# Kernel optimization log

Measured on AMD Instinct MI355X. Metric: run time of the kernel, lower is better.

## Reference

```python
import jax, jax.numpy as jnp
import numpy as np

B, S, HID = 2, 2048, 2048
H, HK, D = 32, 8, 64
N_REP = H // HK
SCALE = D ** -0.5


def setup_inputs() -> dict:
    key = jax.random.key(0)
    ks = jax.random.split(key, 9)
    std = HID ** -0.5
    causal = jnp.tril(jnp.ones((S, S), dtype=bool))
    attention_mask = jnp.where(causal, 0.0, -1e9).astype(jnp.float32)[None, None]  # [1,1,S,S]
    return {
        "hidden_states": jax.random.normal(ks[0], (B, S, HID), jnp.float32),
        "attention_mask": attention_mask,
        "q_w": jax.random.normal(ks[1], (HID, H * D), jnp.float32) * std,
        "q_b": jax.random.normal(ks[2], (H * D,), jnp.float32) * 0.01,
        "k_w": jax.random.normal(ks[3], (HID, HK * D), jnp.float32) * std,
        "k_b": jax.random.normal(ks[4], (HK * D,), jnp.float32) * 0.01,
        "v_w": jax.random.normal(ks[5], (HID, HK * D), jnp.float32) * std,
        "v_b": jax.random.normal(ks[6], (HK * D,), jnp.float32) * 0.01,
        "dense_w": jax.random.normal(ks[7], (HID, HID), jnp.float32) * std,
        "dense_b": jax.random.normal(ks[8], (HID,), jnp.float32) * 0.01,
    }


def reference(hidden_states, attention_mask, q_w, q_b, k_w, k_b, v_w, v_b, dense_w, dense_b):
    b, s, _ = hidden_states.shape
    # projections -> [b, h, s, d]
    q = (hidden_states @ q_w + q_b).reshape(b, s, H, D).transpose(0, 2, 1, 3)
    k = (hidden_states @ k_w + k_b).reshape(b, s, HK, D).transpose(0, 2, 1, 3)
    v = (hidden_states @ v_w + v_b).reshape(b, s, HK, D).transpose(0, 2, 1, 3)
    # GQA: repeat_kv (repeat_interleave along head dim)
    k = jnp.repeat(k, N_REP, axis=1)  # [b, H, s, d]
    v = jnp.repeat(v, N_REP, axis=1)
    # eager attention: full score matrix
    scores = jnp.einsum("bhqd,bhkd->bhqk", q, k) * SCALE + attention_mask
    w = jax.nn.softmax(scores.astype(jnp.float32), axis=-1).astype(q.dtype)
    attn = jnp.einsum("bhqk,bhkd->bhqd", w, v)
    attn = attn.transpose(0, 2, 1, 3).reshape(b, s, H * D)
    return attn @ dense_w + dense_b
```

## Files before the change

kernel.cpp:

```cpp
#include <hip/hip_runtime.h>
#include <hip/hip_bf16.h>


typedef short s16x8 __attribute__((ext_vector_type(8)));
typedef float f32x4 __attribute__((ext_vector_type(4)));

static constexpr int BB = 2, SS = 2048, HID = 2048, HH = 32, HKV = 8, DD = 64;
static constexpr int MM = BB * SS;
static constexpr int NQKV = 3072;

#define DEV __device__ __forceinline__

DEV short f2bf(float f) {
    unsigned u = __builtin_bit_cast(unsigned, f);
    return (short)((u + 0x7fffu + ((u >> 16) & 1u)) >> 16);
}

DEV void stage16(const short* gsrc, short* lbase) {
    __builtin_amdgcn_global_load_lds((const __attribute__((address_space(1))) void*)gsrc,
                                     (__attribute__((address_space(3))) void*)lbase, 16, 0, 0);
}

__global__ __launch_bounds__(256) void cvt_f32_bf16(const float* __restrict__ in,
                                                    short* __restrict__ out, int n) {
    int i = (blockIdx.x * 256 + threadIdx.x) * 8;
    if (i >= n) return;
    float4 a = *reinterpret_cast<const float4*>(in + i);
    float4 b = *reinterpret_cast<const float4*>(in + i + 4);
    s16x8 o;
    o[0] = f2bf(a.x); o[1] = f2bf(a.y); o[2] = f2bf(a.z); o[3] = f2bf(a.w);
    o[4] = f2bf(b.x); o[5] = f2bf(b.y); o[6] = f2bf(b.z); o[7] = f2bf(b.w);
    *reinterpret_cast<s16x8*>(out + i) = o;
}

__global__ __launch_bounds__(256) void transpose_cvt(const float* __restrict__ in,
                                                     short* __restrict__ out,
                                                     int K, int N) {
    __shared__ float tile[32][33];
    int k0 = blockIdx.x * 32, n0 = blockIdx.y * 32;
    int tx = threadIdx.x & 31, ty = threadIdx.x >> 5;
#pragma unroll
    for (int r = ty; r < 32; r += 8)
        tile[r][tx] = in[(size_t)(k0 + r) * N + n0 + tx];
    __syncthreads();
#pragma unroll
    for (int r = ty; r < 32; r += 8)
        out[(size_t)(n0 + r) * K + k0 + tx] = f2bf(tile[tx][r]);
}

__global__ __launch_bounds__(256) void transpose_v(const short* __restrict__ QKV,
                                                   short* __restrict__ Vtg) {
    __shared__ int tile[32][33];
    const int s0 = blockIdx.x * 32, c0 = blockIdx.y * 32, b = blockIdx.z;
    const int tx = threadIdx.x & 31, ty = threadIdx.x >> 5;
#pragma unroll
    for (int r = ty; r < 32; r += 8)
        tile[r][tx] = QKV[(size_t)(b * SS + s0 + r) * NQKV + 2560 + c0 + tx];
    __syncthreads();
#pragma unroll
    for (int r = ty; r < 32; r += 8) {
        const int c = c0 + r;
        Vtg[((size_t)(b * HKV + (c >> 6)) * 64 + (c & 63)) * SS + s0 + tx] = (short)tile[tx][r];
    }
}

__global__ __launch_bounds__(256) void concat_bias(const float* __restrict__ qb,
                                                   const float* __restrict__ kb,
                                                   const float* __restrict__ vb,
                                                   float* __restrict__ cb) {
    int i = blockIdx.x * 256 + threadIdx.x;
    if (i < 2048) cb[i] = qb[i];
    else if (i < 2560) cb[i] = kb[i - 2048];
    else if (i < 3072) cb[i] = vb[i - 2560];
}

template <int BM, int BN, typename OutT>
__global__ __launch_bounds__(512) void gemm8p(const short* __restrict__ A,
                                              const short* __restrict__ Bt,
                                              const float* __restrict__ bias,
                                              OutT* __restrict__ C,
                                              int M, int N, int K, int qcols) {
    constexpr int NR = BN / 64;
    constexpr int ACH = BM * 4;
    constexpr int BCH = BN * 4;
    static_assert(ACH % 512 == 0, "A chunks per half must be thread-uniform");
    constexpr int SA = ACH / 512;
    __shared__ __align__(16) short lds[(BM + BN) * 128];
    const int tid = threadIdx.x, lane = tid & 63, wid = tid >> 6;
    const int fr = lane & 15, fk = lane >> 4;
    const int wm = wid >> 2, wn = wid & 3;
    const int nbn = N / BN;
    const int cpx = gridDim.x >> 3;
    const int wg = (blockIdx.x & 7) * cpx + (blockIdx.x >> 3);
    const int bm = wg / nbn, bn = wg % nbn;
    const int NT = K / 64;

    const short* Ablk = A + (size_t)bm * BM * K;
    const short* Bblk = Bt + (size_t)bn * BN * K;

    auto abase = [&](int bf, int kh) { return bf * (BM * 64) + kh * (BM * 32); };
    auto bbase = [&](int bf, int kh) { return 2 * (BM * 64) + bf * (BN * 64) + kh * (BN * 32); };

    auto stA = [&](int bf, int kh, int kt) {
#pragma unroll
        for (int l = 0; l < SA; ++l) {
            const int c = l * 512 + tid;
            const int r = c >> 2, sg = (c & 3) ^ ((r >> 1) & 3);
            stage16(Ablk + (size_t)r * K + kt + kh * 32 + sg * 8,
                    &lds[abase(bf, kh) + (l * 512 + wid * 64) * 8]);
        }
    };
    auto stB = [&](int bf, int kh, int kt) {
        {
            const int c = tid;
            const int r = c >> 2, sg = (c & 3) ^ ((r >> 1) & 3);
            stage16(Bblk + (size_t)r * K + kt + kh * 32 + sg * 8,
                    &lds[bbase(bf, kh) + (wid * 64) * 8]);
        }
        if constexpr (BCH > 512) {
            if (tid < BCH - 512) {
                const int c = 512 + tid;
                const int r = c >> 2, sg = (c & 3) ^ ((r >> 1) & 3);
                stage16(Bblk + (size_t)r * K + kt + kh * 32 + sg * 8,
                        &lds[bbase(bf, kh) + ((512 + wid * 64)) * 8]);
            }
        }
    };

    auto waithalf = [&](bool pf) {
        if (!pf) { asm volatile("s_waitcnt vmcnt(0)" ::: "memory"); return; }
        if constexpr (BCH > 512) {
            if (wid < (BCH - 512) / 64) asm volatile("s_waitcnt vmcnt(4)" ::: "memory");
            else                        asm volatile("s_waitcnt vmcnt(3)" ::: "memory");
        } else {
            asm volatile("s_waitcnt vmcnt(3)" ::: "memory");
        }
    };

    f32x4 acc[8][NR] = {};

    stA(0, 0, 0); stB(0, 0, 0);
    stA(0, 1, 0); stB(0, 1, 0);
    waithalf(true);
    asm volatile("s_barrier" ::: "memory");

    for (int t = 0; t < NT; ++t) {
        const int bf = t & 1, sf = bf ^ 1;
        const int ktn = (t + 1) * 64;
        const bool pf = (t + 1 < NT);
#pragma unroll
        for (int kh = 0; kh < 2; ++kh) {
            s16x8 bfrag[NR], afrag[8];
#pragma unroll
            for (int n = 0; n < NR; ++n) {
                const int row = wn * (BN / 4) + n * 16 + fr;
                bfrag[n] = *reinterpret_cast<const s16x8*>(
                    &lds[bbase(bf, kh) + row * 32 + ((fk ^ ((row >> 1) & 3)) * 8)]);
            }
#pragma unroll
            for (int i = 0; i < 8; ++i) {
                const int row = wm * 128 + i * 16 + fr;
                afrag[i] = *reinterpret_cast<const s16x8*>(
                    &lds[abase(bf, kh) + row * 32 + ((fk ^ ((row >> 1) & 3)) * 8)]);
            }
            if (pf) stA(sf, kh, ktn);
            __builtin_amdgcn_s_setprio(1);
#pragma unroll
            for (int i = 0; i < 4; ++i)
#pragma unroll
                for (int n = 0; n < NR; ++n)
                    acc[i][n] = __builtin_amdgcn_mfma_f32_16x16x32_bf16(
                        afrag[i], bfrag[n], acc[i][n], 0, 0, 0);
            __builtin_amdgcn_s_setprio(0);
            if (pf) stB(sf, kh, ktn);
            __builtin_amdgcn_s_setprio(1);
#pragma unroll
            for (int i = 4; i < 8; ++i)
#pragma unroll
                for (int n = 0; n < NR; ++n)
                    acc[i][n] = __builtin_amdgcn_mfma_f32_16x16x32_bf16(
                        afrag[i], bfrag[n], acc[i][n], 0, 0, 0);
            __builtin_amdgcn_s_setprio(0);
            waithalf(pf);
            asm volatile("s_barrier" ::: "memory");
        }
    }

#pragma unroll
    for (int n = 0; n < NR; ++n) {
        const int col = bn * BN + wn * (BN / 4) + n * 16 + fr;
        const float bv = bias[col];
        const float sc = (col < qcols) ? 0.125f : 1.0f;
#pragma unroll
        for (int mi = 0; mi < 8; ++mi) {
            const int row0 = bm * BM + wm * 128 + mi * 16 + fk * 4;
#pragma unroll
            for (int r = 0; r < 4; ++r) {
                const float v = (acc[mi][n][r] + bv) * sc;
                if constexpr (sizeof(OutT) == 2)
                    reinterpret_cast<short*>(C)[(size_t)(row0 + r) * N + col] = f2bf(v);
                else
                    reinterpret_cast<float*>(C)[(size_t)(row0 + r) * N + col] = v;
            }
        }
    }
}

__global__ __launch_bounds__(256, 2) void attn_fwd(
        const short* __restrict__ QKV,
        const short* __restrict__ Vtg,
        short* __restrict__ Ob) {
    constexpr int KB = 64;
    __shared__ __align__(16) short Qs[128 * 64];
    __shared__ __align__(16) short Ks[2][KB * 64];
    __shared__ __align__(16) short Vt[2][64 * 64];
    __shared__ __align__(16) short Ps[128 * 64];

    const int pair = blockIdx.x;
    const int bh = blockIdx.y;
    const int b = bh >> 5, h = bh & 31;
    const int kvh = h >> 2;
    const int tid = threadIdx.x, lane = tid & 63, wid = tid >> 6;
    const int fr = lane & 15, fk = lane >> 4;
    const int wq0 = wid * 32;

    const short* kbase = QKV + (size_t)b * SS * NQKV + 2048 + kvh * DD;
    const short* vbase = Vtg + (size_t)(b * HKV + kvh) * 64 * SS;

    auto stageKV = [&](int bb, int kv0) {
#pragma unroll
        for (int is = 0; is < 2; ++is) {
            const int c = is * 256 + wid * 64 + lane;
            const int r = c >> 3, sg = (c & 7) ^ (r & 7);
            stage16(kbase + (size_t)(kv0 + r) * NQKV + sg * 8,
                    &Ks[bb][(is * 256 + wid * 64) * 8]);
            stage16(vbase + (size_t)r * SS + kv0 + sg * 8,
                    &Vt[bb][(is * 256 + wid * 64) * 8]);
        }
    };
    auto stageQ = [&](int q0) {
        const short* qbase = QKV + ((size_t)b * SS + q0) * NQKV + h * DD;
#pragma unroll
        for (int is = 0; is < 4; ++is) {
            const int c = is * 256 + wid * 64 + lane;
            const int r = c >> 3, sg = (c & 7) ^ (r & 7);
            stage16(qbase + (size_t)r * NQKV + sg * 8,
                    &Qs[(is * 256 + wid * 64) * 8]);
        }
    };

    s16x8 ones = {};
    if (fr == 0) {
#pragma unroll
        for (int e = 0; e < 8; ++e) ones[e] = (short)0x3F80;
    }

    int cur = 0;
    stageQ(pair * 128);
    stageKV(0, 0);

    for (int sidx = 0; sidx < 2; ++sidx) {
        const int strip = sidx ? (15 - pair) : pair;
        const int q0 = strip * 128;
        const size_t qrow0 = (size_t)b * SS + q0;
        const int nt = 2 * strip + 2;

        __syncthreads();

        s16x8 aq[2][2];
#pragma unroll
        for (int i = 0; i < 2; ++i)
#pragma unroll
            for (int ks = 0; ks < 2; ++ks) {
                const int row = wq0 + i * 16 + fr;
                const int byte = (ks * 64 + fk * 16) ^ ((row & 7) << 4);
                aq[i][ks] = *reinterpret_cast<const s16x8*>(
                    reinterpret_cast<const char*>(Qs) + row * 128 + byte);
            }

        f32x4 acc_o[2][4] = {};
        f32x4 acc_l[2] = {};

        for (int t = 0; t < nt; ++t) {
            const int kv0 = t * KB;
            if (t + 1 < nt) {
                stageKV(cur ^ 1, kv0 + KB);
            } else if (sidx == 0) {
                stageQ((15 - pair) * 128);
                stageKV(cur ^ 1, 0);
            }

            f32x4 sacc[2][4] = {};
            __builtin_amdgcn_s_setprio(1);
#pragma unroll
            for (int j = 0; j < 4; ++j)
#pragma unroll
                for (int ks = 0; ks < 2; ++ks) {
                    const int row = j * 16 + fr;
                    const int byte = (ks * 64 + fk * 16) ^ ((row & 7) << 4);
                    s16x8 bk = *reinterpret_cast<const s16x8*>(
                        reinterpret_cast<const char*>(Ks[cur]) + row * 128 + byte);
#pragma unroll
                    for (int i = 0; i < 2; ++i)
                        sacc[i][j] = __builtin_amdgcn_mfma_f32_16x16x32_bf16(aq[i][ks], bk, sacc[i][j], 0, 0, 0);
                }
            __builtin_amdgcn_s_setprio(0);

            if (kv0 + KB - 1 > q0 + wq0) {
#pragma unroll
                for (int i = 0; i < 2; ++i) {
                    const int qg = q0 + wq0 + i * 16 + fk * 4;
#pragma unroll
                    for (int j = 0; j < 4; ++j) {
                        const int kvc = kv0 + j * 16 + fr;
#pragma unroll
                        for (int r = 0; r < 4; ++r)
                            if (kvc > qg + r) sacc[i][j][r] = -INFINITY;
                    }
                }
            }

#pragma unroll
            for (int i = 0; i < 2; ++i)
#pragma unroll
                for (int j = 0; j < 4; ++j)
#pragma unroll
                    for (int r = 0; r < 4; ++r) {
                        const int row = wq0 + i * 16 + fk * 4 + r;
                        const int byte = ((j * 16 + fr) * 2) ^ ((row & 7) << 4);
                        *reinterpret_cast<short*>(reinterpret_cast<char*>(Ps) + row * 128 + byte) =
                            f2bf(__expf(sacc[i][j][r]));
                    }

            s16x8 ap[2][2];
#pragma unroll
            for (int i = 0; i < 2; ++i)
#pragma unroll
                for (int ks = 0; ks < 2; ++ks) {
                    const int row = wq0 + i * 16 + fr;
                    const int byte = (ks * 64 + fk * 16) ^ ((row & 7) << 4);
                    ap[i][ks] = *reinterpret_cast<const s16x8*>(
                        reinterpret_cast<const char*>(Ps) + row * 128 + byte);
                }

            __builtin_amdgcn_s_setprio(1);
#pragma unroll
            for (int jd = 0; jd < 4; ++jd)
#pragma unroll
                for (int ks = 0; ks < 2; ++ks) {
                    const int row = jd * 16 + fr;
                    const int byte = (ks * 64 + fk * 16) ^ ((row & 7) << 4);
                    s16x8 bv = *reinterpret_cast<const s16x8*>(
                        reinterpret_cast<const char*>(Vt[cur]) + row * 128 + byte);
#pragma unroll
                    for (int i = 0; i < 2; ++i)
                        acc_o[i][jd] = __builtin_amdgcn_mfma_f32_16x16x32_bf16(ap[i][ks], bv, acc_o[i][jd], 0, 0, 0);
                }
#pragma unroll
            for (int i = 0; i < 2; ++i)
#pragma unroll
                for (int ks = 0; ks < 2; ++ks)
                    acc_l[i] = __builtin_amdgcn_mfma_f32_16x16x32_bf16(ap[i][ks], ones, acc_l[i], 0, 0, 0);
            __builtin_amdgcn_s_setprio(0);

            __syncthreads();
            cur ^= 1;
        }

#pragma unroll
        for (int i = 0; i < 2; ++i)
#pragma unroll
            for (int r = 0; r < 4; ++r) {
                const float l = __shfl(acc_l[i][r], (lane & 48));
                const float inv = 1.f / l;
                const size_t grow = (qrow0 + wq0 + i * 16 + fk * 4 + r) * (size_t)(HH * DD) + h * DD;
#pragma unroll
                for (int jd = 0; jd < 4; ++jd)
                    Ob[grow + jd * 16 + fr] = f2bf(acc_o[i][jd][r] * inv);
            }
    }
}

extern "C" void kernel_launch(void* const* d_in, const int* in_sizes, int n_in,
                              void* d_out, int out_size, void* d_ws, size_t ws_size,
                              hipStream_t stream) {
    const float* hidden  = (const float*)d_in[0];
    const float* q_w     = (const float*)d_in[2];
    const float* q_b     = (const float*)d_in[3];
    const float* k_w     = (const float*)d_in[4];
    const float* k_b     = (const float*)d_in[5];
    const float* v_w     = (const float*)d_in[6];
    const float* v_b     = (const float*)d_in[7];
    const float* dense_w = (const float*)d_in[8];
    const float* dense_b = (const float*)d_in[9];
    float* out = (float*)d_out;

    short* wt   = (short*)d_ws;
    short* dwt  = wt + 6291456;
    short* QKV  = dwt + 4194304;
    short* Vtg  = QKV + 12582912;
    short* hidb = Vtg + 2097152;
    short* Ob   = hidb;
    float* cbias = (float*)(hidb + 8388608);

    cvt_f32_bf16<<<4096, 256, 0, stream>>>(hidden, hidb, MM * HID);
    transpose_cvt<<<dim3(64, 64), 256, 0, stream>>>(q_w, wt, HID, HH * DD);
    transpose_cvt<<<dim3(64, 16), 256, 0, stream>>>(k_w, wt + 2048 * 2048, HID, HKV * DD);
    transpose_cvt<<<dim3(64, 16), 256, 0, stream>>>(v_w, wt + 2560 * 2048, HID, HKV * DD);
    transpose_cvt<<<dim3(64, 64), 256, 0, stream>>>(dense_w, dwt, HID, HID);
    concat_bias<<<12, 256, 0, stream>>>(q_b, k_b, v_b, cbias);

    gemm8p<256, 192, short><<<256, 512, 0, stream>>>(hidb, wt, cbias, QKV, MM, NQKV, HID, 2048);

    transpose_v<<<dim3(64, 16, 2), 256, 0, stream>>>(QKV, Vtg);

    attn_fwd<<<dim3(8, 64), 256, 0, stream>>>(QKV, Vtg, Ob);

    gemm8p<256, 128, float><<<256, 512, 0, stream>>>(Ob, dwt, dense_b, out, MM, HID, HID, 0);
}
```

Measured before the change: 188.5 us.

## Shrink attention query tile to 64 rows with transposed S and packed bf16 P writes

The attention kernel now processes 64-row query strips (16 rows per wave) instead of 128. It launches twice as many blocks and raises the occupancy hint to 3 blocks per CU. The QK^T MFMA is transposed (K as A operand, Q as B) so each lane holds consecutive kv columns. This lets P be written to LDS as packed bf16 pairs via v_cvt_pk_bf16_f32 instead of scalar shorts, and Ps/Qs LDS usage is halved. In exchange, K/V tiles are reloaded from global/L2 twice as often per query row, and each wave has less MFMA work per K/V tile load.

```diff
diff --git a/kernel.cpp b/kernel.cpp
--- a/kernel.cpp
+++ b/kernel.cpp
@@ -14,6 +14,12 @@
 DEV short f2bf(float f) {
     unsigned u = __builtin_bit_cast(unsigned, f);
     return (short)((u + 0x7fffu + ((u >> 16) & 1u)) >> 16);
+}
+
+DEV unsigned cvtpk(float lo, float hi) {
+    unsigned r;
+    asm("v_cvt_pk_bf16_f32 %0, %1, %2" : "=v"(r) : "v"(lo), "v"(hi));
+    return r;
 }
 
 DEV void stage16(const short* gsrc, short* lbase) {
@@ -206,15 +212,15 @@
     }
 }
 
-__global__ __launch_bounds__(256, 2) void attn_fwd(
+__global__ __launch_bounds__(256, 3) void attn_fwd(
         const short* __restrict__ QKV,
         const short* __restrict__ Vtg,
         short* __restrict__ Ob) {
     constexpr int KB = 64;
-    __shared__ __align__(16) short Qs[128 * 64];
+    __shared__ __align__(16) short Qs[64 * 64];
     __shared__ __align__(16) short Ks[2][KB * 64];
     __shared__ __align__(16) short Vt[2][64 * 64];
-    __shared__ __align__(16) short Ps[128 * 64];
+    __shared__ __align__(16) short Ps[4 * 16 * 64];
 
     const int pair = blockIdx.x;
     const int bh = blockIdx.y;
@@ -222,10 +228,11 @@
     const int kvh = h >> 2;
     const int tid = threadIdx.x, lane = tid & 63, wid = tid >> 6;
     const int fr = lane & 15, fk = lane >> 4;
-    const int wq0 = wid * 32;
+    const int wq0 = wid * 16;
 
     const short* kbase = QKV + (size_t)b * SS * NQKV + 2048 + kvh * DD;
     const short* vbase = Vtg + (size_t)(b * HKV + kvh) * 64 * SS;
+    char* pbase = reinterpret_cast<char*>(Ps) + wid * 2048 + fr * 128;
 
     auto stageKV = [&](int bb, int kv0) {
 #pragma unroll
@@ -241,7 +248,7 @@
     auto stageQ = [&](int q0) {
         const short* qbase = QKV + ((size_t)b * SS + q0) * NQKV + h * DD;
 #pragma unroll
-        for (int is = 0; is < 4; ++is) {
+        for (int is = 0; is < 2; ++is) {
             const int c = is * 256 + wid * 64 + lane;
             const int r = c >> 3, sg = (c & 7) ^ (r & 7);
             stage16(qbase + (size_t)r * NQKV + sg * 8,
@@ -256,41 +263,39 @@
     }
 
     int cur = 0;
-    stageQ(pair * 128);
+    stageQ(pair * 64);
     stageKV(0, 0);
 
     for (int sidx = 0; sidx < 2; ++sidx) {
-        const int strip = sidx ? (15 - pair) : pair;
-        const int q0 = strip * 128;
+        const int strip = sidx ? (31 - pair) : pair;
+        const int q0 = strip * 64;
         const size_t qrow0 = (size_t)b * SS + q0;
-        const int nt = 2 * strip + 2;
+        const int nt = strip + 1;
 
         __syncthreads();
 
-        s16x8 aq[2][2];
-#pragma unroll
-        for (int i = 0; i < 2; ++i)
-#pragma unroll
-            for (int ks = 0; ks < 2; ++ks) {
-                const int row = wq0 + i * 16 + fr;
-                const int byte = (ks * 64 + fk * 16) ^ ((row & 7) << 4);
-                aq[i][ks] = *reinterpret_cast<const s16x8*>(
-                    reinterpret_cast<const char*>(Qs) + row * 128 + byte);
-            }
-
-        f32x4 acc_o[2][4] = {};
-        f32x4 acc_l[2] = {};
+        s16x8 bq[2];
+#pragma unroll
+        for (int ks = 0; ks < 2; ++ks) {
+            const int row = wq0 + fr;
+            const int byte = (ks * 64 + fk * 16) ^ ((row & 7) << 4);
+            bq[ks] = *reinterpret_cast<const s16x8*>(
+                reinterpret_cast<const char*>(Qs) + row * 128 + byte);
+        }
+
+        f32x4 acc_o[4] = {};
+        f32x4 acc_l = {};
 
         for (int t = 0; t < nt; ++t) {
             const int kv0 = t * KB;
             if (t + 1 < nt) {
                 stageKV(cur ^ 1, kv0 + KB);
             } else if (sidx == 0) {
-                stageQ((15 - pair) * 128);
+                stageQ((31 - pair) * 64);
                 stageKV(cur ^ 1, 0);
             }
 
-            f32x4 sacc[2][4] = {};
+            f32x4 sacc[4] = {};
             __builtin_amdgcn_s_setprio(1);
 #pragma unroll
             for (int j = 0; j < 4; ++j)
@@ -298,50 +303,39 @@
                 for (int ks = 0; ks < 2; ++ks) {
                     const int row = j * 16 + fr;
                     const int byte = (ks * 64 + fk * 16) ^ ((row & 7) << 4);
-                    s16x8 bk = *reinterpret_cast<const s16x8*>(
+                    s16x8 kf = *reinterpret_cast<const s16x8*>(
                         reinterpret_cast<const char*>(Ks[cur]) + row * 128 + byte);
-#pragma unroll
-                    for (int i = 0; i < 2; ++i)
-                        sacc[i][j] = __builtin_amdgcn_mfma_f32_16x16x32_bf16(aq[i][ks], bk, sacc[i][j], 0, 0, 0);
+                    sacc[j] = __builtin_amdgcn_mfma_f32_16x16x32_bf16(kf, bq[ks], sacc[j], 0, 0, 0);
                 }
             __builtin_amdgcn_s_setprio(0);
 
             if (kv0 + KB - 1 > q0 + wq0) {
-#pragma unroll
-                for (int i = 0; i < 2; ++i) {
-                    const int qg = q0 + wq0 + i * 16 + fk * 4;
-#pragma unroll
-                    for (int j = 0; j < 4; ++j) {
-                        const int kvc = kv0 + j * 16 + fr;
-#pragma unroll
-                        for (int r = 0; r < 4; ++r)
-                            if (kvc > qg + r) sacc[i][j][r] = -INFINITY;
-                    }
+                const int qg = q0 + wq0 + fr;
+#pragma unroll
+                for (int j = 0; j < 4; ++j) {
+                    const int kvb = kv0 + j * 16 + fk * 4;
+#pragma unroll
+                    for (int r = 0; r < 4; ++r)
+                        if (kvb + r > qg) sacc[j][r] = -INFINITY;
                 }
             }
 
 #pragma unroll
-            for (int i = 0; i < 2; ++i)
-#pragma unroll
-                for (int j = 0; j < 4; ++j)
-#pragma unroll
-                    for (int r = 0; r < 4; ++r) {
-                        const int row = wq0 + i * 16 + fk * 4 + r;
-                        const int byte = ((j * 16 + fr) * 2) ^ ((row & 7) << 4);
-                        *reinterpret_cast<short*>(reinterpret_cast<char*>(Ps) + row * 128 + byte) =
-                            f2bf(__expf(sacc[i][j][r]));
-                    }
-
-            s16x8 ap[2][2];
-#pragma unroll
-            for (int i = 0; i < 2; ++i)
-#pragma unroll
-                for (int ks = 0; ks < 2; ++ks) {
-                    const int row = wq0 + i * 16 + fr;
-                    const int byte = (ks * 64 + fk * 16) ^ ((row & 7) << 4);
-                    ap[i][ks] = *reinterpret_cast<const s16x8*>(
-                        reinterpret_cast<const char*>(Ps) + row * 128 + byte);
+            for (int j = 0; j < 4; ++j)
+#pragma unroll
+                for (int hh = 0; hh < 2; ++hh) {
+                    const unsigned pw = cvtpk(__expf(sacc[j][2 * hh]),
+                                              __expf(sacc[j][2 * hh + 1]));
+                    const int byte = ((j * 8 + fk * 2 + hh) << 2) ^ ((fr & 7) << 4);
+                    *reinterpret_cast<unsigned*>(pbase + byte) = pw;
                 }
+
+            s16x8 ap[2];
+#pragma unroll
+            for (int ks = 0; ks < 2; ++ks) {
+                const int byte = ((ks * 4 + fk) * 16) ^ ((fr & 7) << 4);
+                ap[ks] = *reinterpret_cast<const s16x8*>(pbase + byte);
+            }
 
             __builtin_amdgcn_s_setprio(1);
 #pragma unroll
@@ -352,15 +346,11 @@
                     const int byte = (ks * 64 + fk * 16) ^ ((row & 7) << 4);
                     s16x8 bv = *reinterpret_cast<const s16x8*>(
                         reinterpret_cast<const char*>(Vt[cur]) + row * 128 + byte);
-#pragma unroll
-                    for (int i = 0; i < 2; ++i)
-                        acc_o[i][jd] = __builtin_amdgcn_mfma_f32_16x16x32_bf16(ap[i][ks], bv, acc_o[i][jd], 0, 0, 0);
+                    acc_o[jd] = __builtin_amdgcn_mfma_f32_16x16x32_bf16(ap[ks], bv, acc_o[jd], 0, 0, 0);
                 }
 #pragma unroll
-            for (int i = 0; i < 2; ++i)
-#pragma unroll
-                for (int ks = 0; ks < 2; ++ks)
-                    acc_l[i] = __builtin_amdgcn_mfma_f32_16x16x32_bf16(ap[i][ks], ones, acc_l[i], 0, 0, 0);
+            for (int ks = 0; ks < 2; ++ks)
+                acc_l = __builtin_amdgcn_mfma_f32_16x16x32_bf16(ap[ks], ones, acc_l, 0, 0, 0);
             __builtin_amdgcn_s_setprio(0);
 
             __syncthreads();
@@ -368,16 +358,14 @@
         }
 
 #pragma unroll
-        for (int i = 0; i < 2; ++i)
-#pragma unroll
-            for (int r = 0; r < 4; ++r) {
-                const float l = __shfl(acc_l[i][r], (lane & 48));
-                const float inv = 1.f / l;
-                const size_t grow = (qrow0 + wq0 + i * 16 + fk * 4 + r) * (size_t)(HH * DD) + h * DD;
-#pragma unroll
-                for (int jd = 0; jd < 4; ++jd)
-                    Ob[grow + jd * 16 + fr] = f2bf(acc_o[i][jd][r] * inv);
-            }
+        for (int r = 0; r < 4; ++r) {
+            const float l = __shfl(acc_l[r], (lane & 48));
+            const float inv = 1.f / l;
+            const size_t grow = (qrow0 + wq0 + fk * 4 + r) * (size_t)(HH * DD) + h * DD;
+#pragma unroll
+            for (int jd = 0; jd < 4; ++jd)
+                Ob[grow + jd * 16 + fr] = f2bf(acc_o[jd][r] * inv);
+        }
     }
 }
 
@@ -414,7 +402,7 @@
 
     transpose_v<<<dim3(64, 16, 2), 256, 0, stream>>>(QKV, Vtg);
 
-    attn_fwd<<<dim3(8, 64), 256, 0, stream>>>(QKV, Vtg, Ob);
+    attn_fwd<<<dim3(16, 64), 256, 0, stream>>>(QKV, Vtg, Ob);
 
     gemm8p<256, 128, float><<<256, 512, 0, stream>>>(Ob, dwt, dense_b, out, MM, HID, HID, 0);
 }
```

Measured after the change: 194.2 us. +3.0%, slower.
